# Kernel tuning notes

Hardware: AMD Instinct MI355X
Metric: run time of the kernel (lower is better)

The kernel has to match this reference:

```python
import jax, jax.numpy as jnp
import numpy as np

B, H, W, C = 8, 64, 64, 128
L = H * W
NH = 4
HD = C // NH
SCALE = HD ** -0.5
WIN = 8
SHIFT = 4
DEPTH = 2
K = 3
N = WIN * WIN
NW = (H // WIN) * (W // WIN)


def _rel_pos_index(win):
    coords = np.stack(np.meshgrid(np.arange(win), np.arange(win), indexing='ij'))
    cf = coords.reshape(2, -1)
    rel = (cf[:, :, None] - cf[:, None, :]).transpose(1, 2, 0).copy()
    rel[:, :, 0] += win - 1
    rel[:, :, 1] += win - 1
    rel[:, :, 0] *= 2 * win - 1
    return rel.sum(-1)  # (N, N)

REL_IDX = jnp.asarray(_rel_pos_index(WIN).reshape(-1))


def _attn_mask(Hh, Ww, win, shift):
    img = np.zeros((Hh, Ww))
    cnt = 0
    for hs in (slice(0, -win), slice(-win, -shift), slice(-shift, None)):
        for ws in (slice(0, -win), slice(-win, -shift), slice(-shift, None)):
            img[hs, ws] = cnt
            cnt += 1
    mw = img.reshape(Hh // win, win, Ww // win, win).transpose(0, 2, 1, 3).reshape(-1, win * win)
    m = mw[:, None, :] - mw[:, :, None]
    return jnp.asarray(np.where(m != 0, -100.0, 0.0).astype(np.float32))  # (nW, N, N)

ATTN_MASK = _attn_mask(H, W, WIN, SHIFT)


def layer_norm(x, g, b, eps=1e-5):
    mu = x.mean(-1, keepdims=True)
    var = x.var(-1, keepdims=True)
    return (x - mu) / jnp.sqrt(var + eps) * g + b


def window_partition(x, win):
    Bb, Hh, Ww, Cc = x.shape
    x = x.reshape(Bb, Hh // win, win, Ww // win, win, Cc)
    return x.transpose(0, 1, 3, 2, 4, 5).reshape(-1, win, win, Cc)


def window_reverse(wins, win, Hh, Ww):
    Bb = wins.shape[0] // (Hh * Ww // win // win)
    x = wins.reshape(Bb, Hh // win, Ww // win, win, win, -1)
    return x.transpose(0, 1, 3, 2, 4, 5).reshape(Bb, Hh, Ww, -1)


def swin_block(x, shift, n1g, n1b, qkvw, qkvb, rp, pw, pb, n2g, n2b, f1w, f1b, f2w, f2b):
    shortcut = x
    x = layer_norm(x, n1g, n1b).reshape(B, H, W, C)
    if shift > 0:
        x = jnp.roll(x, (-shift, -shift), axis=(1, 2))
    xw = window_partition(x, WIN).reshape(-1, N, C)  # (B*nW, N, C)
    qkv = (xw @ qkvw + qkvb).reshape(-1, N, 3, NH, HD).transpose(2, 0, 3, 1, 4)
    q, k, v = qkv[0] * SCALE, qkv[1], qkv[2]
    attn = jnp.einsum('whnd,whmd->whnm', q, k)  # (B*nW, NH, N, N)
    bias = rp[REL_IDX].reshape(N, N, NH).transpose(2, 0, 1)
    attn = attn + bias[None]
    if shift > 0:
        attn = (attn.reshape(B, NW, NH, N, N) + ATTN_MASK[None, :, None]).reshape(-1, NH, N, N)
    attn = jax.nn.softmax(attn, axis=-1)
    out = jnp.einsum('whnm,whmd->whnd', attn, v).transpose(0, 2, 1, 3).reshape(-1, N, C)
    out = out @ pw + pb
    x = window_reverse(out.reshape(-1, WIN, WIN, C), WIN, H, W)
    if shift > 0:
        x = jnp.roll(x, (shift, shift), axis=(1, 2))
    x = shortcut + x.reshape(B, L, C)
    h = layer_norm(x, n2g, n2b)
    h = jax.nn.gelu(h @ f1w + f1b, approximate=False) @ f2w + f2b
    return x + h


def conv1d(x, w, b):  # x (B,C,L), w (O,I,K)
    y = jax.lax.conv_general_dilated(x, w, (1,), [(K // 2, K // 2)], dimension_numbers=('NCH', 'OIH', 'NCH'))
    return y + b[None, :, None]


def deform_conv1d(xt, off_w, off_b, msk_w, msk_b):
    x = xt.transpose(0, 2, 1)  # (B, C, L)
    offset = conv1d(x, off_w, off_b)                    # (B, K, L)
    mask = jax.nn.sigmoid(conv1d(x, msk_w, msk_b))      # (B, K, L)
    i = jnp.arange(L, dtype=x.dtype)
    pos = jnp.clip(i[None, None, :] + offset, 0.0, L - 1)  # (B, K, L)
    fp = jnp.floor(pos).astype(jnp.int32)
    cp = jnp.minimum(fp + 1, L - 1)
    alpha = pos - fp.astype(x.dtype)
    idx_f = jnp.broadcast_to(fp[:, None], (B, C, K, L))
    idx_c = jnp.broadcast_to(cp[:, None], (B, C, K, L))
    xe = jnp.broadcast_to(x[:, :, None, :], (B, C, K, L))
    xf = jnp.take_along_axis(xe, idx_f, axis=3)
    xc = jnp.take_along_axis(xe, idx_c, axis=3)
    samp = xf * (1.0 - alpha[:, None]) + xc * alpha[:, None]
    out = (samp * mask[:, None]).sum(2)  # (B, C, L)
    # faithful to torch: output.view(B, L, out_channels) reinterprets memory, no transpose
    return out.reshape(B, L, C)


def _forward(xt, hx, cx, red_w, red_b, n1g, n1b, qkvw, qkvb, rp, pw, pb, n2g, n2b,
             f1w, f1b, f2w, f2b, off_w, off_b, msk_w, msk_b, lf_w, lf_b, gf_w, gf_b, ff_w, ff_b):
    # global branch: inject hidden state then W-MSA / SW-MSA blocks
    g = jnp.concatenate([xt, hx], axis=-1) @ red_w + red_b
    for i, shift in enumerate((0, SHIFT)):
        g = swin_block(g, shift, n1g[i], n1b[i], qkvw[i], qkvb[i], rp[i], pw[i], pb[i],
                       n2g[i], n2b[i], f1w[i], f1b[i], f2w[i], f2b[i])
    # local branch: deformable 1D conv over token axis
    local = deform_conv1d(xt, off_w, off_b, msk_w, msk_b)
    # local-global fusion
    fu = jax.nn.relu((local @ lf_w + lf_b) * (g @ gf_w + gf_b)) @ ff_w + ff_b
    # LSTM-style gating (SwinLSTM cell update)
    gate = jax.nn.sigmoid(fu)
    cell = jnp.tanh(fu)
    cy = gate * (cx + cell)
    hy = gate * jnp.tanh(cy)
    return hy


def setup_inputs():
    key = jax.random.key(0)
    ks = iter(jax.random.split(key, 24))
    def rn(shape, s=0.02):
        return jax.random.normal(next(ks), shape, jnp.float32) * s
    return dict(
        xt=jax.random.normal(next(ks), (B, L, C), jnp.float32),
        hx=jax.random.normal(next(ks), (B, L, C), jnp.float32),
        cx=jax.random.normal(next(ks), (B, L, C), jnp.float32),
        red_w=rn((2 * C, C)), red_b=jnp.zeros((C,), jnp.float32),
        n1g=jnp.ones((DEPTH, C), jnp.float32), n1b=jnp.zeros((DEPTH, C), jnp.float32),
        qkvw=rn((DEPTH, C, 3 * C)), qkvb=jnp.zeros((DEPTH, 3 * C), jnp.float32),
        rp=rn((DEPTH, (2 * WIN - 1) ** 2, NH)),
        pw=rn((DEPTH, C, C)), pb=jnp.zeros((DEPTH, C), jnp.float32),
        n2g=jnp.ones((DEPTH, C), jnp.float32), n2b=jnp.zeros((DEPTH, C), jnp.float32),
        f1w=rn((DEPTH, C, 4 * C)), f1b=jnp.zeros((DEPTH, 4 * C), jnp.float32),
        f2w=rn((DEPTH, 4 * C, C)), f2b=jnp.zeros((DEPTH, C), jnp.float32),
        off_w=rn((K, C, K)), off_b=jnp.zeros((K,), jnp.float32),
        msk_w=rn((K, C, K)), msk_b=jnp.zeros((K,), jnp.float32),
        lf_w=rn((C, C)), lf_b=jnp.zeros((C,), jnp.float32),
        gf_w=rn((C, C)), gf_b=jnp.zeros((C,), jnp.float32),
        ff_w=rn((C, C)), ff_b=jnp.zeros((C,), jnp.float32),
    )


def reference(xt, hx, cx, red_w, red_b, n1g, n1b, qkvw, qkvb, rp, pw, pb, n2g, n2b,
              f1w, f1b, f2w, f2b, off_w, off_b, msk_w, msk_b, lf_w, lf_b, gf_w, gf_b, ff_w, ff_b):
    return _forward(xt, hx, cx, red_w, red_b, n1g, n1b, qkvw, qkvb, rp, pw, pb, n2g, n2b,
                    f1w, f1b, f2w, f2b, off_w, off_b, msk_w, msk_b, lf_w, lf_b, gf_w, gf_b, ff_w, ff_b)
```

## Files before the change

### kernel.cpp

```cpp
#include <hip/hip_runtime.h>
#include <hip/hip_bf16.h>
#include <math.h>

typedef __hip_bfloat16 bf16;
typedef unsigned short u16;
#define BF(x) __bfloat162float(x)
static __device__ __forceinline__ bf16 FB(float x) { return __float2bfloat16(x); }
static __device__ __forceinline__ u16 FBu(float x) {
    bf16 b = __float2bfloat16(x);
    return *(u16*)&b;
}

typedef __attribute__((ext_vector_type(4))) float f32x4;
typedef __attribute__((ext_vector_type(8))) __bf16 bf16x8;


#define O_REDW 0
#define O_QKVW 32768
#define O_PW   131072
#define O_F1W  163840
#define O_F2W  294912
#define O_LFW  425984
#define O_GFW  442368
#define O_FFW  458752
#define O_REDB 475136
#define O_QKVB 475264
#define O_PB   476032
#define O_F1B  476288
#define O_F2B  477312
#define O_LFB  477568
#define O_GFB  477696
#define O_FFB  477824
#define O_RP   477952
#define O_N1G  479752
#define O_N1B  480008
#define O_N2G  480264
#define O_N2B  480520
#define O_OW   480776
#define O_OB   481928
#define O_MW   481931
#define O_MB   483083

#define ROW_S 36
#define CH_S  2320

__device__ __forceinline__ int get_mode(const void* xt) {
    const unsigned* w = (const unsigned*)xt;
    int zlo = 0, inband = 0;
    #pragma unroll
    for (int i = 0; i < 32; ++i) {
        unsigned lo = w[i] & 0xFFFFu;
        int e = (int)((lo >> 7) & 0xFF);
        zlo += (lo == 0u || lo == 0x8000u);
        inband += (e >= 100 && e <= 140);
    }
    if (zlo >= 29) return 1;
    return (inband >= 20) ? 0 : 1;
}

__device__ __forceinline__ float LD(const void* p, size_t i, int mode) {
    return mode ? ((const float*)p)[i] : BF(((const bf16*)p)[i]);
}

__device__ __forceinline__ void async16(const u16* g, u16* l) {
    __builtin_amdgcn_global_load_lds(
        (const __attribute__((address_space(1))) unsigned int*)g,
        (__attribute__((address_space(3))) unsigned int*)l, 16, 0, 0);
}

struct PrepT { const void* src; int srcOff, K, N, dstOff; };
struct Prep { PrepT d[29]; int start[30]; };

__global__ void prep_k(Prep p, bf16* __restrict__ dst, const void* __restrict__ dtp) {
    const int mode = get_mode(dtp);
    int i = blockIdx.x * 256 + threadIdx.x;
    if (i >= p.start[29]) return;
    int s = 0;
    while (p.start[s + 1] <= i) ++s;
    int e = i - p.start[s];
    float v;
    if (p.d[s].N > 0) {
        int n = e / p.d[s].K, k = e % p.d[s].K;
        v = LD(p.d[s].src, (size_t)p.d[s].srcOff + (size_t)k * p.d[s].N + n, mode);
    } else {
        v = LD(p.d[s].src, (size_t)p.d[s].srcOff + e, mode);
    }
    dst[p.d[s].dstOff + e] = FB(v);
}

__launch_bounds__(256)
__global__ void xcat_k(const void* __restrict__ xt, const void* __restrict__ hx,
                       u16* __restrict__ X) {
    const int mode = get_mode(xt);
    const int total = 32768 * 32;
    for (int gidx = blockIdx.x * 256 + threadIdx.x; gidx < total;
         gidx += gridDim.x * 256) {
        int r = gidx >> 5, gi = gidx & 31;
        const void* src = (gi < 16) ? xt : hx;
        int c = (gi & 15) << 3;
        u16 outv[8];
        if (mode) {
            const float* s = (const float*)src + (size_t)r * 128 + c;
            float4 a = *(const float4*)s;
            float4 b = *(const float4*)(s + 4);
            outv[0] = FBu(a.x); outv[1] = FBu(a.y); outv[2] = FBu(a.z); outv[3] = FBu(a.w);
            outv[4] = FBu(b.x); outv[5] = FBu(b.y); outv[6] = FBu(b.z); outv[7] = FBu(b.w);
        } else {
            *(uint4*)outv = *(const uint4*)((const u16*)src + (size_t)r * 128 + c);
        }
        *(uint4*)(X + (size_t)r * 256 + (gi << 3)) = *(const uint4*)outv;
    }
}

template <int EPI>
__launch_bounds__(256)
__global__ void gemm_mfma(const u16* __restrict__ A, const u16* __restrict__ Bt,
                          const bf16* __restrict__ bias, bf16* __restrict__ outb,
                          float* __restrict__ outf, int M, int N, int K, int shift) {
    __shared__ __align__(16) u16 Als[2][2048];
    __shared__ __align__(16) u16 Bls[2][4096];
    const int tid = threadIdx.x;
    const int wave = tid >> 6, lane = tid & 63;
    const int q = lane >> 4, lr = lane & 15;
    const int wm = (wave >> 1) << 5, wn = (wave & 1) << 6;
    const int bm = blockIdx.y << 6, bn = blockIdx.x << 7;
    const f32x4 zero = {0.f, 0.f, 0.f, 0.f};
    f32x4 acc[2][4];
    #pragma unroll
    for (int i = 0; i < 2; ++i)
        #pragma unroll
        for (int j = 0; j < 4; ++j) acc[i][j] = zero;

    const int nk = K >> 5;
    {
        int c = tid;
        async16(A + (size_t)(bm + (c >> 2)) * K + ((c & 3) << 3), Als[0] + (c << 3));
        #pragma unroll
        for (int c2 = tid; c2 < 512; c2 += 256)
            async16(Bt + (size_t)(bn + (c2 >> 2)) * K + ((c2 & 3) << 3), Bls[0] + (c2 << 3));
    }
    __syncthreads();

    for (int i = 0; i < nk; ++i) {
        const int cur = i & 1, nxt = cur ^ 1;
        if (i + 1 < nk) {
            int k1 = (i + 1) << 5;
            int c = tid;
            async16(A + (size_t)(bm + (c >> 2)) * K + k1 + ((c & 3) << 3), Als[nxt] + (c << 3));
            #pragma unroll
            for (int c2 = tid; c2 < 512; c2 += 256)
                async16(Bt + (size_t)(bn + (c2 >> 2)) * K + k1 + ((c2 & 3) << 3), Bls[nxt] + (c2 << 3));
        }
        bf16x8 af[2], bfr[4];
        #pragma unroll
        for (int t = 0; t < 2; ++t)
            af[t] = *(const bf16x8*)(Als[cur] + ((wm + (t << 4) + lr) << 5) + (q << 3));
        #pragma unroll
        for (int t = 0; t < 4; ++t)
            bfr[t] = *(const bf16x8*)(Bls[cur] + ((wn + (t << 4) + lr) << 5) + (q << 3));
        #pragma unroll
        for (int mt = 0; mt < 2; ++mt)
            #pragma unroll
            for (int nt = 0; nt < 4; ++nt)
                acc[mt][nt] = __builtin_amdgcn_mfma_f32_16x16x32_bf16(
                    af[mt], bfr[nt], acc[mt][nt], 0, 0, 0);
        __syncthreads();
    }

    #pragma unroll
    for (int nt = 0; nt < 4; ++nt) {
        int col = bn + wn + (nt << 4) + lr;
        float bv = BF(bias[col]);
        #pragma unroll
        for (int mt = 0; mt < 2; ++mt) {
            int row0 = bm + wm + (mt << 4) + (q << 2);
            #pragma unroll
            for (int i = 0; i < 4; ++i) {
                int r = row0 + i;
                float v = acc[mt][nt][i] + bv;
                size_t idx = (size_t)r * N + col;
                if (EPI == 0) {
                    outb[idx] = FB(v);
                } else if (EPI == 3) {
                    int b = r >> 12, rem = r & 4095;
                    int wi = rem >> 6, n = rem & 63;
                    int hp = ((wi >> 3) << 3) + (n >> 3);
                    int wp = ((wi & 7) << 3) + (n & 7);
                    int h = (hp + shift) & 63, w = (wp + shift) & 63;
                    outf[((size_t)((b << 12) + (h << 6) + w)) * 128 + col] += v;
                } else if (EPI == 5) {
                    outf[idx] = v;
                }
            }
        }
    }
}

__launch_bounds__(256)
__global__ void qkvln_k(const float* __restrict__ g, const u16* __restrict__ wtu,
                        const bf16* __restrict__ wtb, u16* __restrict__ qkv,
                        int d, int shift) {
    __shared__ __align__(16) u16 Ach[4 * CH_S];
    __shared__ __align__(16) u16 Bb[2][8192];
    const int tid = threadIdx.x;
    const int wave = tid >> 6, lane = tid & 63;
    const int q = lane >> 4, lr = lane & 15;
    const int wm = (wave >> 1) << 5, wn = (wave & 1) << 6;
    const int bm = blockIdx.x << 6;
    const u16* Wq = wtu + O_QKVW + d * 49152;

    #pragma unroll
    for (int i = tid; i < 1024; i += 256) {
        int kc = i >> 9, c = i & 511;
        async16(Wq + (size_t)(c >> 2) * 128 + (kc << 5) + ((c & 3) << 3),
                Bb[0] + (kc << 12) + (c << 3));
    }

    {
        int row = tid >> 2, qtr = tid & 3;
        int r = bm + row;
        int b = r >> 12, rem = r & 4095;
        int wi = rem >> 6, n = rem & 63;
        int hp = ((wi >> 3) << 3) + (n >> 3);
        int wp = ((wi & 7) << 3) + (n & 7);
        int h = (hp + shift) & 63, w = (wp + shift) & 63;
        int src = (b << 12) + (h << 6) + w;
        const float* gr = g + (size_t)src * 128 + qtr * 32;
        float vals[32];
        float s1 = 0.f, s2 = 0.f;
        #pragma unroll
        for (int i = 0; i < 8; ++i) {
            float4 v4 = *(const float4*)(gr + i * 4);
            vals[i * 4] = v4.x; vals[i * 4 + 1] = v4.y;
            vals[i * 4 + 2] = v4.z; vals[i * 4 + 3] = v4.w;
            s1 += v4.x + v4.y + v4.z + v4.w;
            s2 += v4.x * v4.x + v4.y * v4.y + v4.z * v4.z + v4.w * v4.w;
        }
        s1 += __shfl_xor(s1, 1); s1 += __shfl_xor(s1, 2);
        s2 += __shfl_xor(s2, 1); s2 += __shfl_xor(s2, 2);
        float mu = s1 * (1.f / 128.f);
        float var = s2 * (1.f / 128.f) - mu * mu;
        float inv = rsqrtf(var + 1e-5f);
        #pragma unroll
        for (int i = 0; i < 32; ++i) {
            int c = qtr * 32 + i;
            float o = (vals[i] - mu) * inv * BF(wtb[O_N1G + d * 128 + c])
                      + BF(wtb[O_N1B + d * 128 + c]);
            Ach[qtr * CH_S + row * ROW_S + i] = FBu(o);
        }
    }
    __syncthreads();

    const f32x4 zero = {0.f, 0.f, 0.f, 0.f};
    f32x4 acc[2][4];
    for (int s = 0; s < 6; ++s) {
        const int nc = s >> 1, kh = s & 1;
        const int bsel = s & 1;
        if (s < 5) {
            int t = s + 1, nct = t >> 1, kht = t & 1;
            const u16* Bg = Wq + nct * 16384;
            #pragma unroll
            for (int i = tid; i < 1024; i += 256) {
                int kc = i >> 9, c = i & 511;
                async16(Bg + (size_t)(c >> 2) * 128 + (kht << 6) + (kc << 5) + ((c & 3) << 3),
                        Bb[t & 1] + (kc << 12) + (c << 3));
            }
        }
        if (kh == 0) {
            #pragma unroll
            for (int i = 0; i < 2; ++i)
                #pragma unroll
                for (int j = 0; j < 4; ++j) acc[i][j] = zero;
        }
        #pragma unroll
        for (int kc = 0; kc < 2; ++kc) {
            bf16x8 af[2], bfr[4];
            #pragma unroll
            for (int t = 0; t < 2; ++t)
                af[t] = *(const bf16x8*)(Ach + (2 * kh + kc) * CH_S + (wm + (t << 4) + lr) * ROW_S + (q << 3));
            #pragma unroll
            for (int t = 0; t < 4; ++t)
                bfr[t] = *(const bf16x8*)(Bb[bsel] + (kc << 12) + ((wn + (t << 4) + lr) << 5) + (q << 3));
            #pragma unroll
            for (int mt = 0; mt < 2; ++mt)
                #pragma unroll
                for (int nt = 0; nt < 4; ++nt)
                    acc[mt][nt] = __builtin_amdgcn_mfma_f32_16x16x32_bf16(
                        af[mt], bfr[nt], acc[mt][nt], 0, 0, 0);
        }
        if (kh == 1) {
            #pragma unroll
            for (int nt = 0; nt < 4; ++nt) {
                int col = wn + (nt << 4) + lr;
                float bv = BF(wtb[O_QKVB + d * 384 + nc * 128 + col]);
                #pragma unroll
                for (int mt = 0; mt < 2; ++mt) {
                    #pragma unroll
                    for (int i = 0; i < 4; ++i) {
                        int r = bm + wm + (mt << 4) + (q << 2) + i;
                        qkv[(size_t)r * 384 + nc * 128 + col] = FBu(acc[mt][nt][i] + bv);
                    }
                }
            }
        }
        if (s < 5) __syncthreads();
    }
}

__launch_bounds__(256)
__global__ void attn_k(const u16* __restrict__ qkv, const bf16* __restrict__ rp,
                       u16* __restrict__ outp, int shift) {
    __shared__ float kT[4][32][64];
    __shared__ float vT[4][32][64];
    const int wq = blockIdx.x;
    const int head = threadIdx.x >> 6;
    const int t = threadIdx.x & 63;
    const size_t rbase = (size_t)(wq * 64 + t) * 384 + head * 32;
    float q[32];
    #pragma unroll
    for (int j = 0; j < 4; ++j) {
        bf16x8 qv = *(const bf16x8*)(qkv + rbase + j * 8);
        bf16x8 kv = *(const bf16x8*)(qkv + rbase + 128 + j * 8);
        bf16x8 vv = *(const bf16x8*)(qkv + rbase + 256 + j * 8);
        #pragma unroll
        for (int e = 0; e < 8; ++e) {
            int dd = j * 8 + e;
            q[dd] = (float)qv[e] * 0.17677669529663687f;
            kT[head][dd][t] = (float)kv[e];
            vT[head][dd][t] = (float)vv[e];
        }
    }
    __syncthreads();
    const int wloc = wq & 63;
    const int wh = (wloc >> 3) << 3, wwb = (wloc & 7) << 3;
    int regt = 0;
    if (shift) {
        int hp = wh + (t >> 3), wp = wwb + (t & 7);
        int rh = hp < 56 ? 0 : (hp < 60 ? 1 : 2);
        int rw = wp < 56 ? 0 : (wp < 60 ? 1 : 2);
        regt = rh * 3 + rw;
    }
    const int ti = t >> 3, tj = t & 7;
    float s[64];
    float mx = -1e30f;
    #pragma unroll
    for (int m = 0; m < 64; ++m) {
        float acc = 0.f;
        #pragma unroll
        for (int dd = 0; dd < 32; ++dd) acc += q[dd] * kT[head][dd][m];
        int idx = (ti - (m >> 3) + 7) * 15 + (tj - (m & 7) + 7);
        acc += BF(rp[idx * 4 + head]);
        if (shift) {
            int hp = wh + (m >> 3), wp = wwb + (m & 7);
            int rh = hp < 56 ? 0 : (hp < 60 ? 1 : 2);
            int rw = wp < 56 ? 0 : (wp < 60 ? 1 : 2);
            if (regt != rh * 3 + rw) acc -= 100.f;
        }
        s[m] = acc;
        mx = fmaxf(mx, acc);
    }
    float l = 0.f;
    #pragma unroll
    for (int m = 0; m < 64; ++m) {
        s[m] = expf(s[m] - mx);
        l += s[m];
    }
    const float inv = 1.f / l;
    const size_t obase = (size_t)(wq * 64 + t) * 128 + head * 32;
    #pragma unroll
    for (int j = 0; j < 4; ++j) {
        bf16x8 ov;
        #pragma unroll
        for (int e = 0; e < 8; ++e) {
            int dd = j * 8 + e;
            float a = 0.f;
            #pragma unroll
            for (int m = 0; m < 64; ++m) a += s[m] * vT[head][dd][m];
            ov[e] = (__bf16)(a * inv);
        }
        *(bf16x8*)(outp + obase + j * 8) = ov;
    }
}

__launch_bounds__(256)
__global__ void mlp_k(float* __restrict__ g, bf16* __restrict__ gbf,
                      const u16* __restrict__ wtu, const bf16* __restrict__ wtb,
                      int d) {
    __shared__ __align__(16) u16 Ach[4 * CH_S];
    __shared__ __align__(16) u16 bufB1[8192];
    __shared__ __align__(16) u16 bufB2[8192];
    __shared__ __align__(16) u16 buf2[2 * CH_S];
    const int tid = threadIdx.x;
    const int wave = tid >> 6, lane = tid & 63;
    const int q = lane >> 4, lr = lane & 15;
    const int wm = (wave >> 1) << 5;
    const int wn0 = (wave & 1) << 5;
    const int wn = (wave & 1) << 6;
    const int bm = blockIdx.x << 6;

    {
        const u16* B1g = wtu + O_F1W + d * 65536;
        #pragma unroll
        for (int i = tid; i < 1024; i += 256) {
            int kc = i >> 8, c = i & 255;
            async16(B1g + (c >> 2) * 128 + (kc << 5) + ((c & 3) << 3),
                    bufB1 + (kc << 11) + (c << 3));
        }
    }

    {
        int row = tid >> 2, qtr = tid & 3;
        const float* gr = g + (size_t)(bm + row) * 128 + qtr * 32;
        float vals[32];
        float s1 = 0.f, s2 = 0.f;
        #pragma unroll
        for (int i = 0; i < 8; ++i) {
            float4 v4 = *(const float4*)(gr + i * 4);
            vals[i * 4] = v4.x; vals[i * 4 + 1] = v4.y;
            vals[i * 4 + 2] = v4.z; vals[i * 4 + 3] = v4.w;
            s1 += v4.x + v4.y + v4.z + v4.w;
            s2 += v4.x * v4.x + v4.y * v4.y + v4.z * v4.z + v4.w * v4.w;
        }
        s1 += __shfl_xor(s1, 1); s1 += __shfl_xor(s1, 2);
        s2 += __shfl_xor(s2, 1); s2 += __shfl_xor(s2, 2);
        float mu = s1 * (1.f / 128.f);
        float var = s2 * (1.f / 128.f) - mu * mu;
        float inv = rsqrtf(var + 1e-5f);
        #pragma unroll
        for (int i = 0; i < 32; ++i) {
            int c = qtr * 32 + i;
            float o = (vals[i] - mu) * inv * BF(wtb[O_N2G + d * 128 + c])
                      + BF(wtb[O_N2B + d * 128 + c]);
            Ach[qtr * CH_S + row * ROW_S + i] = FBu(o);
        }
    }
    __syncthreads();

    const f32x4 zero = {0.f, 0.f, 0.f, 0.f};
    f32x4 acc2[2][4];
    #pragma unroll
    for (int i = 0; i < 2; ++i)
        #pragma unroll
        for (int j = 0; j < 4; ++j) acc2[i][j] = zero;

    for (int h = 0; h < 8; ++h) {
        {
            const u16* B2g = wtu + O_F2W + d * 65536 + h * 64;
            #pragma unroll
            for (int i = tid; i < 1024; i += 256) {
                int kc = i >> 9, c = i & 511;
                async16(B2g + (size_t)(c >> 2) * 512 + (kc << 5) + ((c & 3) << 3),
                        bufB2 + (kc << 12) + (c << 3));
            }
        }
        f32x4 acc1[2][2];
        #pragma unroll
        for (int i = 0; i < 2; ++i) { acc1[i][0] = zero; acc1[i][1] = zero; }
        #pragma unroll
        for (int k0 = 0; k0 < 4; ++k0) {
            bf16x8 af[2], bfr[2];
            #pragma unroll
            for (int t = 0; t < 2; ++t) {
                af[t]  = *(const bf16x8*)(Ach + k0 * CH_S + (wm + (t << 4) + lr) * ROW_S + (q << 3));
                bfr[t] = *(const bf16x8*)(bufB1 + (k0 << 11) + ((wn0 + (t << 4) + lr) << 5) + (q << 3));
            }
            #pragma unroll
            for (int mt = 0; mt < 2; ++mt)
                #pragma unroll
                for (int nt = 0; nt < 2; ++nt)
                    acc1[mt][nt] = __builtin_amdgcn_mfma_f32_16x16x32_bf16(
                        af[mt], bfr[nt], acc1[mt][nt], 0, 0, 0);
        }
        #pragma unroll
        for (int nt = 0; nt < 2; ++nt) {
            int c = wn0 + (nt << 4) + lr;
            float hb = BF(wtb[O_F1B + d * 512 + h * 64 + c]);
            #pragma unroll
            for (int mt = 0; mt < 2; ++mt) {
                #pragma unroll
                for (int i = 0; i < 4; ++i) {
                    int r = wm + (mt << 4) + (q << 2) + i;
                    float v = acc1[mt][nt][i] + hb;
                    float ge = 0.5f * v * (1.0f + erff(v * 0.70710678118654752f));
                    buf2[(c >> 5) * CH_S + r * ROW_S + (c & 31)] = FBu(ge);
                }
            }
        }
        __syncthreads();
        if (h < 7) {
            const u16* B1g = wtu + O_F1W + d * 65536 + (h + 1) * 8192;
            #pragma unroll
            for (int i = tid; i < 1024; i += 256) {
                int kc = i >> 8, c = i & 255;
                async16(B1g + (c >> 2) * 128 + (kc << 5) + ((c & 3) << 3),
                        bufB1 + (kc << 11) + (c << 3));
            }
        }
        #pragma unroll
        for (int kc = 0; kc < 2; ++kc) {
            bf16x8 ah[2], b2[4];
            #pragma unroll
            for (int t = 0; t < 2; ++t)
                ah[t] = *(const bf16x8*)(buf2 + kc * CH_S + (wm + (t << 4) + lr) * ROW_S + (q << 3));
            #pragma unroll
            for (int t = 0; t < 4; ++t)
                b2[t] = *(const bf16x8*)(bufB2 + (kc << 12) + ((wn + (t << 4) + lr) << 5) + (q << 3));
            #pragma unroll
            for (int mt = 0; mt < 2; ++mt)
                #pragma unroll
                for (int nt = 0; nt < 4; ++nt)
                    acc2[mt][nt] = __builtin_amdgcn_mfma_f32_16x16x32_bf16(
                        ah[mt], b2[nt], acc2[mt][nt], 0, 0, 0);
        }
        __syncthreads();
    }
    #pragma unroll
    for (int nt = 0; nt < 4; ++nt) {
        int col = wn + (nt << 4) + lr;
        float bv = BF(wtb[O_F2B + d * 128 + col]);
        #pragma unroll
        for (int mt = 0; mt < 2; ++mt) {
            #pragma unroll
            for (int i = 0; i < 4; ++i) {
                int r = bm + wm + (mt << 4) + (q << 2) + i;
                size_t idx = (size_t)r * 128 + col;
                float nv = g[idx] + acc2[mt][nt][i] + bv;
                g[idx] = nv;
                gbf[idx] = FB(nv);
            }
        }
    }
}

__launch_bounds__(256, 2)
__global__ void fuse3_k(const u16* __restrict__ Aloc, const u16* __restrict__ Ag,
                        const u16* __restrict__ wtu, const bf16* __restrict__ wtb,
                        const void* __restrict__ cx, void* __restrict__ out,
                        const void* __restrict__ dtp) {
    __shared__ __align__(16) u16 relb[4 * CH_S];
    const int mode = get_mode(dtp);
    const int tid = threadIdx.x;
    const int wave = tid >> 6, lane = tid & 63;
    const int q = lane >> 4, lr = lane & 15;
    const int wm = (wave >> 1) << 5, wn = (wave & 1) << 6;
    const int bm = blockIdx.x << 6;
    const f32x4 zero = {0.f, 0.f, 0.f, 0.f};
    f32x4 acc1[2][4], acc2[2][4];
    #pragma unroll
    for (int i = 0; i < 2; ++i)
        #pragma unroll
        for (int j = 0; j < 4; ++j) { acc1[i][j] = zero; acc2[i][j] = zero; }

    #pragma unroll
    for (int k0 = 0; k0 < 4; ++k0) {
        bf16x8 al[2], ag[2], blf[4], bgf[4];
        #pragma unroll
        for (int t = 0; t < 2; ++t) {
            size_t off = (size_t)(bm + wm + (t << 4) + lr) * 128 + (k0 << 5) + (q << 3);
            al[t] = *(const bf16x8*)(Aloc + off);
            ag[t] = *(const bf16x8*)(Ag + off);
        }
        #pragma unroll
        for (int t = 0; t < 4; ++t) {
            int woff = ((wn + (t << 4) + lr) << 7) + (k0 << 5) + (q << 3);
            blf[t] = *(const bf16x8*)(wtu + O_LFW + woff);
            bgf[t] = *(const bf16x8*)(wtu + O_GFW + woff);
        }
        #pragma unroll
        for (int mt = 0; mt < 2; ++mt)
            #pragma unroll
            for (int nt = 0; nt < 4; ++nt) {
                acc1[mt][nt] = __builtin_amdgcn_mfma_f32_16x16x32_bf16(
                    al[mt], blf[nt], acc1[mt][nt], 0, 0, 0);
                acc2[mt][nt] = __builtin_amdgcn_mfma_f32_16x16x32_bf16(
                    ag[mt], bgf[nt], acc2[mt][nt], 0, 0, 0);
            }
    }
    #pragma unroll
    for (int nt = 0; nt < 4; ++nt) {
        int c = wn + (nt << 4) + lr;
        float lfb = BF(wtb[O_LFB + c]);
        float gfb = BF(wtb[O_GFB + c]);
        #pragma unroll
        for (int mt = 0; mt < 2; ++mt) {
            #pragma unroll
            for (int i = 0; i < 4; ++i) {
                int r = wm + (mt << 4) + (q << 2) + i;
                float t1 = acc1[mt][nt][i] + lfb;
                float t2 = acc2[mt][nt][i] + gfb;
                float rel = t1 * t2;
                relb[(c >> 5) * CH_S + r * ROW_S + (c & 31)] = FBu(rel > 0.f ? rel : 0.f);
            }
        }
    }
    __syncthreads();
    f32x4 acc3[2][4];
    #pragma unroll
    for (int i = 0; i < 2; ++i)
        #pragma unroll
        for (int j = 0; j < 4; ++j) acc3[i][j] = zero;
    #pragma unroll
    for (int k0 = 0; k0 < 4; ++k0) {
        bf16x8 ar[2], bff[4];
        #pragma unroll
        for (int t = 0; t < 2; ++t)
            ar[t] = *(const bf16x8*)(relb + k0 * CH_S + (wm + (t << 4) + lr) * ROW_S + (q << 3));
        #pragma unroll
        for (int t = 0; t < 4; ++t)
            bff[t] = *(const bf16x8*)(wtu + O_FFW + ((wn + (t << 4) + lr) << 7) + (k0 << 5) + (q << 3));
        #pragma unroll
        for (int mt = 0; mt < 2; ++mt)
            #pragma unroll
            for (int nt = 0; nt < 4; ++nt)
                acc3[mt][nt] = __builtin_amdgcn_mfma_f32_16x16x32_bf16(
                    ar[mt], bff[nt], acc3[mt][nt], 0, 0, 0);
    }
    #pragma unroll
    for (int nt = 0; nt < 4; ++nt) {
        int col = wn + (nt << 4) + lr;
        float ffb = BF(wtb[O_FFB + col]);
        #pragma unroll
        for (int mt = 0; mt < 2; ++mt) {
            #pragma unroll
            for (int i = 0; i < 4; ++i) {
                int r = bm + wm + (mt << 4) + (q << 2) + i;
                size_t idx = (size_t)r * 128 + col;
                float v = acc3[mt][nt][i] + ffb;
                float gate = 1.f / (1.f + expf(-v));
                float cell = tanhf(v);
                float cy = gate * (LD(cx, idx, mode) + cell);
                float hy = gate * tanhf(cy);
                if (mode) ((float*)out)[idx] = hy;
                else      ((bf16*)out)[idx] = FB(hy);
            }
        }
    }
}

__launch_bounds__(256)
__global__ void offmask_k(const void* __restrict__ xt, const bf16* __restrict__ wtb,
                          float4* __restrict__ om) {
    const int mode = get_mode(xt);
    const int wave = threadIdx.x >> 6, lane = threadIdx.x & 63;
    const int gl = blockIdx.x * 4 + wave;
    const int b = gl >> 12, l = gl & 4095;
    float wo[3][3][2], wmk[3][3][2];
    #pragma unroll
    for (int k = 0; k < 3; ++k)
        #pragma unroll
        for (int j = 0; j < 3; ++j) {
            wo[k][j][0]  = BF(wtb[O_OW + (k * 128 + lane) * 3 + j]);
            wo[k][j][1]  = BF(wtb[O_OW + (k * 128 + lane + 64) * 3 + j]);
            wmk[k][j][0] = BF(wtb[O_MW + (k * 128 + lane) * 3 + j]);
            wmk[k][j][1] = BF(wtb[O_MW + (k * 128 + lane + 64) * 3 + j]);
        }
    float a6[6] = {};
    #pragma unroll
    for (int j = 0; j < 3; ++j) {
        int row = l + j - 1;
        if (row >= 0 && row < 4096) {
            size_t base = ((size_t)(b << 12) + row) * 128;
            float x0 = LD(xt, base + lane, mode);
            float x1 = LD(xt, base + lane + 64, mode);
            #pragma unroll
            for (int k = 0; k < 3; ++k) {
                a6[k]     += x0 * wo[k][j][0]  + x1 * wo[k][j][1];
                a6[3 + k] += x0 * wmk[k][j][0] + x1 * wmk[k][j][1];
            }
        }
    }
    #pragma unroll
    for (int off = 32; off > 0; off >>= 1)
        #pragma unroll
        for (int k = 0; k < 6; ++k) a6[k] += __shfl_down(a6[k], off);
    if (lane == 0) {
        #pragma unroll
        for (int k = 0; k < 3; ++k) {
            float off = a6[k] + BF(wtb[O_OB + k]);
            float pos = fminf(fmaxf((float)l + off, 0.f), 4095.f);
            float fpf = floorf(pos);
            float mv = a6[3 + k] + BF(wtb[O_MB + k]);
            float mk = 1.f / (1.f + expf(-mv));
            om[(size_t)gl * 3 + k] = make_float4(fpf, pos - fpf, mk, 0.f);
        }
    }
}

__launch_bounds__(512)
__global__ void sample_k(const void* __restrict__ xt, const float4* __restrict__ om,
                         bf16* __restrict__ outL) {
    __shared__ __align__(16) u16 ot[128 * 72];
    const int mode = get_mode(xt);
    const int tid = threadIdx.x;
    const int b = blockIdx.x >> 6;
    const int l0 = (blockIdx.x & 63) << 6;
    const int c = tid & 127, lh = tid >> 7;
    for (int it = 0; it < 16; ++it) {
        int l_loc = lh * 16 + it;
        size_t gl = (size_t)(b << 12) + l0 + l_loc;
        float o = 0.f;
        #pragma unroll
        for (int k = 0; k < 3; ++k) {
            float4 v = om[gl * 3 + k];
            int fp = (int)v.x;
            int cp = fp + 1 > 4095 ? 4095 : fp + 1;
            float al = v.y, mk = v.z;
            float xf = LD(xt, ((size_t)(b << 12) + fp) * 128 + c, mode);
            float xc = LD(xt, ((size_t)(b << 12) + cp) * 128 + c, mode);
            o += (xf * (1.f - al) + xc * al) * mk;
        }
        ot[c * 72 + l_loc] = FBu(o);
    }
    __syncthreads();
    #pragma unroll
    for (int pass = 0; pass < 2; ++pass) {
        int cc = pass * 64 + (tid >> 3);
        int oo = tid & 7;
        const uint4 v = *(const uint4*)(ot + cc * 72 + oo * 8);
        *(uint4*)(outL + (size_t)b * 524288 + (size_t)cc * 4096 + l0 + oo * 8) = v;
    }
}

extern "C" void kernel_launch(void* const* d_in, const int* in_sizes, int n_in,
                              void* d_out, int out_size, void* d_ws, size_t ws_size,
                              hipStream_t stream) {
    (void)out_size; (void)ws_size;
    int I[28] = {0,1,2,3,4,5,6,7,8,9,10,11,12,13,14,15,16,17,18,19,20,21,22,23,24,25,26,27};
    if (n_in >= 28 && in_sizes[7] != 98304 && in_sizes[23] == 98304 && in_sizes[26] == 1800) {
        int alt[28] = {27, 9, 0, 25, 24, 15, 14, 23, 22, 26, 21, 20, 17, 16,
                       2, 1, 4, 3, 19, 18, 13, 12, 11, 10, 8, 7, 6, 5};
        for (int i = 0; i < 28; ++i) I[i] = alt[i];
    }
    const void* xt = d_in[I[0]];
    const void* hx = d_in[I[1]];
    const void* cx = d_in[I[2]];

    char* wsb = (char*)d_ws;
    float* g    = (float*)wsb;
    u16*   Abf  = (u16*)(wsb + 16777216);
    u16*   Bbf  = (u16*)(wsb + 25165824);
    u16*   Cbf  = (u16*)(wsb + 50331648);
    bf16*  wtb  = (bf16*)(wsb + 58720256);
    u16*   wtu  = (u16*)wtb;
    float4* om  = (float4*)(wsb + 25165824);

    Prep p;
    PrepT descs[29] = {
        {d_in[I[3]],  0,     256, 128, O_REDW},
        {d_in[I[7]],  0,     128, 384, O_QKVW},
        {d_in[I[7]],  49152, 128, 384, O_QKVW + 49152},
        {d_in[I[10]], 0,     128, 128, O_PW},
        {d_in[I[10]], 16384, 128, 128, O_PW + 16384},
        {d_in[I[14]], 0,     128, 512, O_F1W},
        {d_in[I[14]], 65536, 128, 512, O_F1W + 65536},
        {d_in[I[16]], 0,     512, 128, O_F2W},
        {d_in[I[16]], 65536, 512, 128, O_F2W + 65536},
        {d_in[I[22]], 0,     128, 128, O_LFW},
        {d_in[I[24]], 0,     128, 128, O_GFW},
        {d_in[I[26]], 0,     128, 128, O_FFW},
        {d_in[I[4]],  0,  128, 0, O_REDB},
        {d_in[I[8]],  0,  768, 0, O_QKVB},
        {d_in[I[11]], 0,  256, 0, O_PB},
        {d_in[I[15]], 0, 1024, 0, O_F1B},
        {d_in[I[17]], 0,  256, 0, O_F2B},
        {d_in[I[23]], 0,  128, 0, O_LFB},
        {d_in[I[25]], 0,  128, 0, O_GFB},
        {d_in[I[27]], 0,  128, 0, O_FFB},
        {d_in[I[9]],  0, 1800, 0, O_RP},
        {d_in[I[5]],  0,  256, 0, O_N1G},
        {d_in[I[6]],  0,  256, 0, O_N1B},
        {d_in[I[12]], 0,  256, 0, O_N2G},
        {d_in[I[13]], 0,  256, 0, O_N2B},
        {d_in[I[18]], 0, 1152, 0, O_OW},
        {d_in[I[19]], 0,    3, 0, O_OB},
        {d_in[I[20]], 0, 1152, 0, O_MW},
        {d_in[I[21]], 0,    3, 0, O_MB},
    };
    int cum = 0;
    for (int i = 0; i < 29; ++i) {
        p.d[i] = descs[i];
        p.start[i] = cum;
        cum += (descs[i].N > 0) ? descs[i].K * descs[i].N : descs[i].K;
    }
    p.start[29] = cum;

    prep_k<<<(cum + 255) / 256, 256, 0, stream>>>(p, wtb, xt);
    xcat_k<<<1024, 256, 0, stream>>>(xt, hx, Bbf);

    gemm_mfma<5><<<dim3(1, 512), 256, 0, stream>>>(Bbf, wtu + O_REDW, wtb + O_REDB,
                                                   nullptr, g, 32768, 128, 256, 0);

    for (int d = 0; d < 2; ++d) {
        int shift = d ? 4 : 0;
        qkvln_k<<<512, 256, 0, stream>>>(g, wtu, wtb, Bbf, d, shift);
        attn_k<<<512, 256, 0, stream>>>(Bbf, wtb + O_RP + d * 900, Cbf, shift);
        gemm_mfma<3><<<dim3(1, 512), 256, 0, stream>>>(Cbf, wtu + O_PW + d * 16384,
                                                       wtb + O_PB + d * 128, nullptr, g,
                                                       32768, 128, 128, shift);
        mlp_k<<<512, 256, 0, stream>>>(g, (bf16*)Abf, wtu, wtb, d);
    }

    offmask_k<<<8192, 256, 0, stream>>>(xt, wtb, om);
    sample_k<<<512, 512, 0, stream>>>(xt, om, (bf16*)Cbf);
    fuse3_k<<<512, 256, 0, stream>>>(Cbf, Abf, wtu, wtb, cx, d_out, xt);
}
```

Baseline: 445.0 us.

## Use MFMA for window attention QK^T and PV in attn_k

Rewrites the window attention kernel so each wave computes QK^T and P·V with bf16 16x16x32 MFMA instructions instead of per-thread scalar FP32 dot products. Softmax is now done on the MFMA accumulator layout using cross-lane shuffles, and probabilities are staged as bf16 in LDS for the second matmul. LDS storage switches from FP32 to padded bf16, and launch bounds request two blocks per CU. The aim is to cut ALU and LDS load work; the cost is rounding the probabilities to bf16 before the PV product.

```diff
diff --git a/kernel.cpp b/kernel.cpp
--- a/kernel.cpp
+++ b/kernel.cpp
@@ -307,79 +307,119 @@
     }
 }
 
-__launch_bounds__(256)
+__launch_bounds__(256, 2)
 __global__ void attn_k(const u16* __restrict__ qkv, const bf16* __restrict__ rp,
                        u16* __restrict__ outp, int shift) {
-    __shared__ float kT[4][32][64];
-    __shared__ float vT[4][32][64];
+    __shared__ __align__(16) u16 vT[4][32][72];
+    __shared__ __align__(16) u16 pbuf[4][64][72];
     const int wq = blockIdx.x;
     const int head = threadIdx.x >> 6;
-    const int t = threadIdx.x & 63;
-    const size_t rbase = (size_t)(wq * 64 + t) * 384 + head * 32;
-    float q[32];
+    const int lane = threadIdx.x & 63;
+    const int q8 = lane >> 4, lr = lane & 15;
+    const size_t base = (size_t)wq * 64;
+    const f32x4 zero = {0.f, 0.f, 0.f, 0.f};
+
     #pragma unroll
     for (int j = 0; j < 4; ++j) {
-        bf16x8 qv = *(const bf16x8*)(qkv + rbase + j * 8);
-        bf16x8 kv = *(const bf16x8*)(qkv + rbase + 128 + j * 8);
-        bf16x8 vv = *(const bf16x8*)(qkv + rbase + 256 + j * 8);
-        #pragma unroll
-        for (int e = 0; e < 8; ++e) {
-            int dd = j * 8 + e;
-            q[dd] = (float)qv[e] * 0.17677669529663687f;
-            kT[head][dd][t] = (float)kv[e];
-            vT[head][dd][t] = (float)vv[e];
-        }
-    }
-    __syncthreads();
+        bf16x8 vv = *(const bf16x8*)(qkv + (base + lane) * 384 + 256 + head * 32 + j * 8);
+        #pragma unroll
+        for (int e = 0; e < 8; ++e) vT[head][j * 8 + e][lane] = ((const u16*)&vv)[e];
+    }
+
+    bf16x8 af[4], bfk[4];
+    #pragma unroll
+    for (int t = 0; t < 4; ++t) {
+        af[t]  = *(const bf16x8*)(qkv + (base + t * 16 + lr) * 384 + head * 32 + q8 * 8);
+        bfk[t] = *(const bf16x8*)(qkv + (base + t * 16 + lr) * 384 + 128 + head * 32 + q8 * 8);
+    }
+    f32x4 accs[4][4];
+    #pragma unroll
+    for (int rt = 0; rt < 4; ++rt)
+        #pragma unroll
+        for (int ct = 0; ct < 4; ++ct) accs[rt][ct] = zero;
+    #pragma unroll
+    for (int rt = 0; rt < 4; ++rt)
+        #pragma unroll
+        for (int ct = 0; ct < 4; ++ct)
+            accs[rt][ct] = __builtin_amdgcn_mfma_f32_16x16x32_bf16(
+                af[rt], bfk[ct], accs[rt][ct], 0, 0, 0);
+
     const int wloc = wq & 63;
     const int wh = (wloc >> 3) << 3, wwb = (wloc & 7) << 3;
-    int regt = 0;
-    if (shift) {
-        int hp = wh + (t >> 3), wp = wwb + (t & 7);
-        int rh = hp < 56 ? 0 : (hp < 60 ? 1 : 2);
-        int rw = wp < 56 ? 0 : (wp < 60 ? 1 : 2);
-        regt = rh * 3 + rw;
-    }
-    const int ti = t >> 3, tj = t & 7;
-    float s[64];
-    float mx = -1e30f;
-    #pragma unroll
-    for (int m = 0; m < 64; ++m) {
-        float acc = 0.f;
-        #pragma unroll
-        for (int dd = 0; dd < 32; ++dd) acc += q[dd] * kT[head][dd][m];
-        int idx = (ti - (m >> 3) + 7) * 15 + (tj - (m & 7) + 7);
-        acc += BF(rp[idx * 4 + head]);
-        if (shift) {
-            int hp = wh + (m >> 3), wp = wwb + (m & 7);
-            int rh = hp < 56 ? 0 : (hp < 60 ? 1 : 2);
-            int rw = wp < 56 ? 0 : (wp < 60 ? 1 : 2);
-            if (regt != rh * 3 + rw) acc -= 100.f;
-        }
-        s[m] = acc;
-        mx = fmaxf(mx, acc);
-    }
-    float l = 0.f;
-    #pragma unroll
-    for (int m = 0; m < 64; ++m) {
-        s[m] = expf(s[m] - mx);
-        l += s[m];
-    }
-    const float inv = 1.f / l;
-    const size_t obase = (size_t)(wq * 64 + t) * 128 + head * 32;
-    #pragma unroll
-    for (int j = 0; j < 4; ++j) {
-        bf16x8 ov;
-        #pragma unroll
-        for (int e = 0; e < 8; ++e) {
-            int dd = j * 8 + e;
-            float a = 0.f;
-            #pragma unroll
-            for (int m = 0; m < 64; ++m) a += s[m] * vT[head][dd][m];
-            ov[e] = (__bf16)(a * inv);
-        }
-        *(bf16x8*)(outp + obase + j * 8) = ov;
-    }
+    #pragma unroll
+    for (int rt = 0; rt < 4; ++rt) {
+        #pragma unroll
+        for (int i = 0; i < 4; ++i) {
+            int r = rt * 16 + q8 * 4 + i;
+            int ti = r >> 3, tj = r & 7;
+            int regt = 0;
+            if (shift) {
+                int hp = wh + ti, wp = wwb + tj;
+                int rh = hp < 56 ? 0 : (hp < 60 ? 1 : 2);
+                int rw = wp < 56 ? 0 : (wp < 60 ? 1 : 2);
+                regt = rh * 3 + rw;
+            }
+            float sv[4];
+            float mx = -1e30f;
+            #pragma unroll
+            for (int ct = 0; ct < 4; ++ct) {
+                int m = ct * 16 + lr;
+                float a = accs[rt][ct][i] * 0.17677669529663687f;
+                int idx = (ti - (m >> 3) + 7) * 15 + (tj - (m & 7) + 7);
+                a += BF(rp[idx * 4 + head]);
+                if (shift) {
+                    int hp = wh + (m >> 3), wp = wwb + (m & 7);
+                    int rh = hp < 56 ? 0 : (hp < 60 ? 1 : 2);
+                    int rw = wp < 56 ? 0 : (wp < 60 ? 1 : 2);
+                    if (regt != rh * 3 + rw) a -= 100.f;
+                }
+                sv[ct] = a;
+                mx = fmaxf(mx, a);
+            }
+            mx = fmaxf(mx, __shfl_xor(mx, 1));
+            mx = fmaxf(mx, __shfl_xor(mx, 2));
+            mx = fmaxf(mx, __shfl_xor(mx, 4));
+            mx = fmaxf(mx, __shfl_xor(mx, 8));
+            float l = 0.f;
+            #pragma unroll
+            for (int ct = 0; ct < 4; ++ct) { sv[ct] = expf(sv[ct] - mx); l += sv[ct]; }
+            l += __shfl_xor(l, 1); l += __shfl_xor(l, 2);
+            l += __shfl_xor(l, 4); l += __shfl_xor(l, 8);
+            float inv = 1.f / l;
+            #pragma unroll
+            for (int ct = 0; ct < 4; ++ct)
+                pbuf[head][r][ct * 16 + lr] = FBu(sv[ct] * inv);
+        }
+    }
+
+    f32x4 acco[4][2];
+    #pragma unroll
+    for (int rt = 0; rt < 4; ++rt) { acco[rt][0] = zero; acco[rt][1] = zero; }
+    #pragma unroll
+    for (int mh = 0; mh < 2; ++mh) {
+        bf16x8 vb[2];
+        #pragma unroll
+        for (int dt = 0; dt < 2; ++dt)
+            vb[dt] = *(const bf16x8*)(&vT[head][dt * 16 + lr][mh * 32 + q8 * 8]);
+        #pragma unroll
+        for (int rt = 0; rt < 4; ++rt) {
+            bf16x8 pa = *(const bf16x8*)(&pbuf[head][rt * 16 + lr][mh * 32 + q8 * 8]);
+            #pragma unroll
+            for (int dt = 0; dt < 2; ++dt)
+                acco[rt][dt] = __builtin_amdgcn_mfma_f32_16x16x32_bf16(
+                    pa, vb[dt], acco[rt][dt], 0, 0, 0);
+        }
+    }
+
+    #pragma unroll
+    for (int rt = 0; rt < 4; ++rt)
+        #pragma unroll
+        for (int dt = 0; dt < 2; ++dt)
+            #pragma unroll
+            for (int i = 0; i < 4; ++i) {
+                int r = rt * 16 + q8 * 4 + i;
+                outp[(base + r) * 128 + head * 32 + dt * 16 + lr] = FBu(acco[rt][dt][i]);
+            }
 }
 
 __launch_bounds__(256)
```

New measurement: 540.7 us. 21.5% more time.
